# Performance work log

Measured on AMD Instinct MI355X. Metric: run time of the kernel, lower is better.

The kernel has to match this reference:

```python
import jax, jax.numpy as jnp
import numpy as np
from jax.scipy.special import logsumexp

REG_E = 0.05      # entropic regularization (init_kwargs reg_e)
N_ITER = 100      # n_iter_sinkhorn
N, M = 4096, 4096


def setup_inputs() -> dict:
    key = jax.random.key(0)
    k1, k2, k3 = jax.random.split(key, 3)
    p = jax.random.uniform(k1, (N,), dtype=jnp.float32)
    p = p / p.sum()                      # probability weights of measure P
    q = jax.random.uniform(k2, (M,), dtype=jnp.float32)
    q = q / q.sum()                      # probability weights of measure Q
    C = jax.random.uniform(k3, (N, M), dtype=jnp.float32)  # ground cost
    return {"p": p, "q": q, "C": C}


def reference(p, q, C):
    # POT ot.bregman.sinkhorn(..., method='sinkhorn_log') on C / C.max()
    # Log-domain Sinkhorn: Mr = -(C/max(C))/reg; alternate potential updates
    #   u = log p - logsumexp(Mr + v[None,:], axis=1)
    #   v = log q - logsumexp(Mr + u[:,None], axis=0)
    # plan = exp(Mr + u[:,None] + v[None,:])
    Mr = -(C / jax.lax.stop_gradient(jnp.max(C))) / REG_E   # (n, m)
    logp = jnp.log(p)
    logq = jnp.log(q)

    def body(_, uv):
        u, v = uv
        u = logp - logsumexp(Mr + v[None, :], axis=1)   # row logsumexp
        v = logq - logsumexp(Mr + u[:, None], axis=0)   # col logsumexp
        return (u, v)

    u0 = jnp.zeros_like(p)
    v0 = jnp.zeros_like(q)
    u, v = jax.lax.fori_loop(0, N_ITER, body, (u0, v0))
    return jnp.exp(Mr + u[:, None] + v[None, :])        # OT plan (n, m)
```

## Files before the change

### kernel.cpp

```cpp
#include <hip/hip_runtime.h>

#define N 4096
#define NITER 100
#define DSTEP (20.0f / 65535.0f)
#define LOG2E 1.44269504088896340736f
#define DSTEP2 (DSTEP * LOG2E)
#define TOL 3e-4f
#define NB 256
#define NT 1024
#define ROWS 16
#define TILE_BYTES (ROWS * N * 2)

typedef unsigned short u16;

__device__ __forceinline__ float aload(const float* p) {
    return __hip_atomic_load(p, __ATOMIC_RELAXED, __HIP_MEMORY_SCOPE_AGENT);
}
__device__ __forceinline__ void astore(float* p, float x) {
    __hip_atomic_store(p, x, __ATOMIC_RELAXED, __HIP_MEMORY_SCOPE_AGENT);
}
__device__ __forceinline__ int aloadi(const int* p) {
    return __hip_atomic_load(p, __ATOMIC_RELAXED, __HIP_MEMORY_SCOPE_AGENT);
}

__device__ __forceinline__ float fexp2(float x) {
#if __has_builtin(__builtin_amdgcn_exp2f)
    return __builtin_amdgcn_exp2f(x);
#else
    return __expf(x * 0.6931471805599453f);
#endif
}

__device__ __forceinline__ void gbar(int* bar, int slot) {
    __syncthreads();
    if (threadIdx.x == 0) {
        __hip_atomic_fetch_add(&bar[slot], 1, __ATOMIC_RELEASE, __HIP_MEMORY_SCOPE_AGENT);
        while (__hip_atomic_load(&bar[slot], __ATOMIC_ACQUIRE, __HIP_MEMORY_SCOPE_AGENT) < NB)
            __builtin_amdgcn_s_sleep(1);
    }
    __syncthreads();
}

__global__ __launch_bounds__(NT) void ot_all(const float* __restrict__ p,
                                             const float* __restrict__ q,
                                             const float* __restrict__ C,
                                             int* maxC,
                                             int* bar,
                                             float* v,
                                             float* part,
                                             float* ddel,
                                             float* __restrict__ out) {
    extern __shared__ u16 tile[];
    const int t = threadIdx.x;
    const int b = blockIdx.x;
    const int lane = t & 63;
    const int wave = t >> 6;
    const int gid = b * NT + t;
    const int r0 = b * ROWS;
    const int c0 = b * 16;
    const int j0 = t * 4;
    int slot = 0;

    __shared__ float sred[4][16];
    __shared__ float wbc[4];
    __shared__ float s2[16][16];
    __shared__ float dm[16];
    __shared__ float wm[16];
    __shared__ float lp[ROWS], pp[ROWS], lq[16], su[ROWS];

    {
        const float4* Crow = (const float4*)(C + (size_t)r0 * N);
        float m = 0.f;
        for (int i = t; i < ROWS * N / 4; i += NT) {
            float4 c = Crow[i];
            m = fmaxf(m, fmaxf(fmaxf(c.x, c.y), fmaxf(c.z, c.w)));
        }
#pragma unroll
        for (int off = 32; off; off >>= 1) m = fmaxf(m, __shfl_down(m, off));
        if (lane == 0) wm[wave] = m;
        __syncthreads();
        if (t == 0) {
            m = wm[0];
#pragma unroll
            for (int i = 1; i < 16; ++i) m = fmaxf(m, wm[i]);
            atomicMax(maxC, __float_as_int(m));
        }
    }
    gbar(bar, slot++);
    const float qmul = 65535.0f / __int_as_float(aloadi(maxC));

    {
        const float4* Crow = (const float4*)(C + (size_t)r0 * N);
        uint2* T2 = (uint2*)tile;
        for (int i = t; i < ROWS * N / 4; i += NT) {
            float4 a = Crow[i];
            uint2 o;
            o.x = min(65535u, __float2uint_rn(a.x * qmul)) | (min(65535u, __float2uint_rn(a.y * qmul)) << 16);
            o.y = min(65535u, __float2uint_rn(a.z * qmul)) | (min(65535u, __float2uint_rn(a.w * qmul)) << 16);
            T2[i] = o;
        }
        if (t < ROWS) {
            float pv = p[r0 + t];
            pp[t] = pv;
            lp[t] = __logf(pv);
            lq[t] = __logf(q[c0 + t]);
            su[t] = 0.f;
        }
        if (gid < N) astore(&v[gid], 0.f);
    }
    float vreg = 0.f;
    gbar(bar, slot++);

    for (int it = 0; it < NITER; ++it) {
        float vv2[4];
#pragma unroll
        for (int k = 0; k < 4; ++k) vv2[k] = aload(&v[j0 + k]) * LOG2E;
        float ca[4] = {0.f, 0.f, 0.f, 0.f};

        for (int ch = 0; ch < 4; ++ch) {
            const int rl = ch * 4;
            float tq[4][4], sp[4];
#pragma unroll
            for (int r = 0; r < 4; ++r) {
                uint2 a = *(const uint2*)(tile + (size_t)(rl + r) * N + j0);
                float e0 = fexp2(fmaf((float)(a.x & 0xffffu), -DSTEP2, vv2[0]));
                float e1 = fexp2(fmaf((float)(a.x >> 16),     -DSTEP2, vv2[1]));
                float e2 = fexp2(fmaf((float)(a.y & 0xffffu), -DSTEP2, vv2[2]));
                float e3 = fexp2(fmaf((float)(a.y >> 16),     -DSTEP2, vv2[3]));
                tq[r][0] = e0; tq[r][1] = e1; tq[r][2] = e2; tq[r][3] = e3;
                sp[r] = (e0 + e1) + (e2 + e3);
            }
#pragma unroll
            for (int r = 0; r < 4; ++r) {
                float s = sp[r];
#pragma unroll
                for (int off = 32; off; off >>= 1) s += __shfl_down(s, off);
                if (lane == 0) sred[r][wave] = s;
            }
            __syncthreads();
            if (wave < 4) {
                float s = (lane < 16) ? sred[wave][lane] : 0.f;
                s += __shfl_down(s, 8);
                s += __shfl_down(s, 4);
                s += __shfl_down(s, 2);
                s += __shfl_down(s, 1);
                if (lane == 0) {
                    wbc[wave] = pp[rl + wave] / s;
                    su[rl + wave] = lp[rl + wave] - __logf(s);
                }
            }
            __syncthreads();
#pragma unroll
            for (int r = 0; r < 4; ++r) {
                const float w = wbc[r];
#pragma unroll
                for (int k = 0; k < 4; ++k) ca[k] = fmaf(tq[r][k], w, ca[k]);
            }
        }
#pragma unroll
        for (int k = 0; k < 4; ++k) astore(&part[(size_t)b * N + j0 + k], ca[k]);
        gbar(bar, slot++);

        {
            const int cl = t & 15;
            const int ch = t >> 4;
            const int c = c0 + cl;
            float s = 0.f;
#pragma unroll
            for (int k = 0; k < 4; ++k) s += aload(&part[(size_t)(ch + 64 * k) * N + c]);
            s += __shfl_down(s, 16);
            s += __shfl_down(s, 32);
            if (lane < 16) s2[cl][wave] = s;
            __syncthreads();
            if (t < 16) {
                float tot = 0.f;
#pragma unroll
                for (int w = 0; w < 16; ++w) tot += s2[t][w];
                const float vn = lq[t] + vreg - __logf(tot);
                astore(&v[c0 + t], vn);
                float d = fabsf(vn - vreg);
                vreg = vn;
                d = fmaxf(d, __shfl_down(d, 8));
                d = fmaxf(d, __shfl_down(d, 4));
                d = fmaxf(d, __shfl_down(d, 2));
                d = fmaxf(d, __shfl_down(d, 1));
                if (t == 0) astore(&ddel[b], d);
            }
        }
        gbar(bar, slot++);

        {
            float d = aload(&ddel[t & 255]);
#pragma unroll
            for (int off = 32; off; off >>= 1) d = fmaxf(d, __shfl_down(d, off));
            if (lane == 0) dm[wave] = d;
            __syncthreads();
            float m = dm[0];
#pragma unroll
            for (int w = 1; w < 16; ++w) m = fmaxf(m, dm[w]);
            __syncthreads();
            if (m < TOL) break;
        }
    }

    {
        float vvl[4];
#pragma unroll
        for (int k = 0; k < 4; ++k) vvl[k] = aload(&v[j0 + k]) * LOG2E;
#pragma unroll 4
        for (int r = 0; r < ROWS; ++r) {
            const float uul = su[r] * LOG2E;
            uint2 a = *(const uint2*)(tile + (size_t)r * N + j0);
            float4 o;
            o.x = fexp2(fmaf((float)(a.x & 0xffffu), -DSTEP2, uul + vvl[0]));
            o.y = fexp2(fmaf((float)(a.x >> 16),     -DSTEP2, uul + vvl[1]));
            o.z = fexp2(fmaf((float)(a.y & 0xffffu), -DSTEP2, uul + vvl[2]));
            o.w = fexp2(fmaf((float)(a.y >> 16),     -DSTEP2, uul + vvl[3]));
            *(float4*)(out + (size_t)(r0 + r) * N + j0) = o;
        }
    }
}

extern "C" void kernel_launch(void* const* d_in, const int* in_sizes, int n_in,
                              void* d_out, int out_size, void* d_ws, size_t ws_size,
                              hipStream_t stream) {
    const float* p = (const float*)d_in[0];
    const float* q = (const float*)d_in[1];
    const float* C = (const float*)d_in[2];
    float* out = (float*)d_out;

    float* W = (float*)d_ws;
    int* maxC = (int*)W;
    int* bar = (int*)(W + 16);
    float* v = W + 512;
    float* ddel = v + N;
    float* part = (float*)((char*)d_ws + 128 * 1024);

    hipMemsetAsync(d_ws, 0, 2048, stream);

    hipFuncSetAttribute((const void*)ot_all, hipFuncAttributeMaxDynamicSharedMemorySize, TILE_BYTES);

    void* args[] = {(void*)&p, (void*)&q, (void*)&C, (void*)&maxC, (void*)&bar,
                    (void*)&v, (void*)&part, (void*)&ddel, (void*)&out};
    hipLaunchCooperativeKernel((void*)ot_all, dim3(NB), dim3(NT), args, TILE_BYTES, stream);
}
```

Before: 205.9 us.

## Use hierarchical grid barriers and overlap max-reduction with tile quantization

Replaces the flat single-counter grid barrier with a two-level barrier: blocks arrive on per-group counters and the last arriver of each group bumps a root counter. Every barrier event now gets its own counters, so the per-iteration ddel slots need no reuse hazard. The first barrier is split into arrive and wait so each block can quantize its C rows with its local max while other blocks finish. The global max is folded into the dequantization step afterwards. This also trims some intra-block syncs in the convergence check, at the cost of a larger workspace memset and more counter memory.

```diff
diff --git a/kernel.cpp b/kernel.cpp
--- a/kernel.cpp
+++ b/kernel.cpp
@@ -2,14 +2,15 @@
 
 #define N 4096
 #define NITER 100
-#define DSTEP (20.0f / 65535.0f)
 #define LOG2E 1.44269504088896340736f
-#define DSTEP2 (DSTEP * LOG2E)
 #define TOL 3e-4f
 #define NB 256
 #define NT 1024
 #define ROWS 16
 #define TILE_BYTES (ROWS * N * 2)
+#define GRPS 8
+#define BPG 32
+#define EVSTRIDE 144
 
 typedef unsigned short u16;
 
@@ -18,9 +19,6 @@
 }
 __device__ __forceinline__ void astore(float* p, float x) {
     __hip_atomic_store(p, x, __ATOMIC_RELAXED, __HIP_MEMORY_SCOPE_AGENT);
-}
-__device__ __forceinline__ int aloadi(const int* p) {
-    return __hip_atomic_load(p, __ATOMIC_RELAXED, __HIP_MEMORY_SCOPE_AGENT);
 }
 
 __device__ __forceinline__ float fexp2(float x) {
@@ -31,24 +29,32 @@
 #endif
 }
 
-__device__ __forceinline__ void gbar(int* bar, int slot) {
-    __syncthreads();
-    if (threadIdx.x == 0) {
-        __hip_atomic_fetch_add(&bar[slot], 1, __ATOMIC_RELEASE, __HIP_MEMORY_SCOPE_AGENT);
-        while (__hip_atomic_load(&bar[slot], __ATOMIC_ACQUIRE, __HIP_MEMORY_SCOPE_AGENT) < NB)
-            __builtin_amdgcn_s_sleep(1);
-    }
+__device__ __forceinline__ void gbar_arrive(int* bar, int e) {
+    int* base = bar + e * EVSTRIDE;
+    const int g = (int)(blockIdx.x >> 5);
+    int r = __hip_atomic_fetch_add(base + g * 16, 1, __ATOMIC_ACQ_REL, __HIP_MEMORY_SCOPE_AGENT);
+    if (r == BPG - 1)
+        __hip_atomic_fetch_add(base + 128, 1, __ATOMIC_ACQ_REL, __HIP_MEMORY_SCOPE_AGENT);
+}
+__device__ __forceinline__ void gbar_wait(int* bar, int e) {
+    const int* root = bar + e * EVSTRIDE + 128;
+    while (__hip_atomic_load(root, __ATOMIC_ACQUIRE, __HIP_MEMORY_SCOPE_AGENT) < GRPS)
+        __builtin_amdgcn_s_sleep(1);
+}
+__device__ __forceinline__ void gbar(int* bar, int e) {
+    __syncthreads();
+    if (threadIdx.x == 0) { gbar_arrive(bar, e); gbar_wait(bar, e); }
     __syncthreads();
 }
 
 __global__ __launch_bounds__(NT) void ot_all(const float* __restrict__ p,
                                              const float* __restrict__ q,
                                              const float* __restrict__ C,
-                                             int* maxC,
                                              int* bar,
+                                             float* fmax_arr,
+                                             float* ddel,
                                              float* v,
                                              float* part,
-                                             float* ddel,
                                              float* __restrict__ out) {
     extern __shared__ u16 tile[];
     const int t = threadIdx.x;
@@ -59,15 +65,15 @@
     const int r0 = b * ROWS;
     const int c0 = b * 16;
     const int j0 = t * 4;
-    int slot = 0;
 
     __shared__ float sred[4][16];
     __shared__ float wbc[4];
     __shared__ float s2[16][16];
     __shared__ float dm[16];
-    __shared__ float wm[16];
     __shared__ float lp[ROWS], pp[ROWS], lq[16], su[ROWS];
-
+    __shared__ float sMown, sMaxC, sM;
+
+    if (gid < N) astore(&v[gid], 0.f);
     {
         const float4* Crow = (const float4*)(C + (size_t)r0 * N);
         float m = 0.f;
@@ -77,19 +83,21 @@
         }
 #pragma unroll
         for (int off = 32; off; off >>= 1) m = fmaxf(m, __shfl_down(m, off));
-        if (lane == 0) wm[wave] = m;
+        if (lane == 0) dm[wave] = m;
         __syncthreads();
         if (t == 0) {
-            m = wm[0];
-#pragma unroll
-            for (int i = 1; i < 16; ++i) m = fmaxf(m, wm[i]);
-            atomicMax(maxC, __float_as_int(m));
-        }
-    }
-    gbar(bar, slot++);
-    const float qmul = 65535.0f / __int_as_float(aloadi(maxC));
+            m = dm[0];
+#pragma unroll
+            for (int i = 1; i < 16; ++i) m = fmaxf(m, dm[i]);
+            sMown = m;
+            astore(&fmax_arr[b], m);
+            gbar_arrive(bar, 0);
+        }
+        __syncthreads();
+    }
 
     {
+        const float qmul = 65535.0f / sMown;
         const float4* Crow = (const float4*)(C + (size_t)r0 * N);
         uint2* T2 = (uint2*)tile;
         for (int i = t; i < ROWS * N / 4; i += NT) {
@@ -106,10 +114,20 @@
             lq[t] = __logf(q[c0 + t]);
             su[t] = 0.f;
         }
-        if (gid < N) astore(&v[gid], 0.f);
-    }
+    }
+    __syncthreads();
+    if (t == 0) gbar_wait(bar, 0);
+    __syncthreads();
+    if (wave == 0) {
+        float d = fmaxf(fmaxf(aload(&fmax_arr[lane]), aload(&fmax_arr[64 + lane])),
+                        fmaxf(aload(&fmax_arr[128 + lane]), aload(&fmax_arr[192 + lane])));
+#pragma unroll
+        for (int off = 32; off; off >>= 1) d = fmaxf(d, __shfl_down(d, off));
+        if (lane == 0) sMaxC = d;
+    }
+    __syncthreads();
+    const float ndstep = -(20.0f / 65535.0f) * (sMown / sMaxC) * LOG2E;
     float vreg = 0.f;
-    gbar(bar, slot++);
 
     for (int it = 0; it < NITER; ++it) {
         float vv2[4];
@@ -123,10 +141,10 @@
 #pragma unroll
             for (int r = 0; r < 4; ++r) {
                 uint2 a = *(const uint2*)(tile + (size_t)(rl + r) * N + j0);
-                float e0 = fexp2(fmaf((float)(a.x & 0xffffu), -DSTEP2, vv2[0]));
-                float e1 = fexp2(fmaf((float)(a.x >> 16),     -DSTEP2, vv2[1]));
-                float e2 = fexp2(fmaf((float)(a.y & 0xffffu), -DSTEP2, vv2[2]));
-                float e3 = fexp2(fmaf((float)(a.y >> 16),     -DSTEP2, vv2[3]));
+                float e0 = fexp2(fmaf((float)(a.x & 0xffffu), ndstep, vv2[0]));
+                float e1 = fexp2(fmaf((float)(a.x >> 16),     ndstep, vv2[1]));
+                float e2 = fexp2(fmaf((float)(a.y & 0xffffu), ndstep, vv2[2]));
+                float e3 = fexp2(fmaf((float)(a.y >> 16),     ndstep, vv2[3]));
                 tq[r][0] = e0; tq[r][1] = e1; tq[r][2] = e2; tq[r][3] = e3;
                 sp[r] = (e0 + e1) + (e2 + e3);
             }
@@ -159,7 +177,7 @@
         }
 #pragma unroll
         for (int k = 0; k < 4; ++k) astore(&part[(size_t)b * N + j0 + k], ca[k]);
-        gbar(bar, slot++);
+        gbar(bar, 1 + 2 * it);
 
         {
             const int cl = t & 15;
@@ -184,23 +202,21 @@
                 d = fmaxf(d, __shfl_down(d, 4));
                 d = fmaxf(d, __shfl_down(d, 2));
                 d = fmaxf(d, __shfl_down(d, 1));
-                if (t == 0) astore(&ddel[b], d);
-            }
-        }
-        gbar(bar, slot++);
-
-        {
-            float d = aload(&ddel[t & 255]);
+                if (t == 0) astore(&ddel[it * NB + b], d);
+            }
+        }
+        gbar(bar, 2 + 2 * it);
+
+        if (wave == 0) {
+            const float* dd = ddel + it * NB;
+            float d = fmaxf(fmaxf(aload(dd + lane), aload(dd + 64 + lane)),
+                            fmaxf(aload(dd + 128 + lane), aload(dd + 192 + lane)));
 #pragma unroll
             for (int off = 32; off; off >>= 1) d = fmaxf(d, __shfl_down(d, off));
-            if (lane == 0) dm[wave] = d;
-            __syncthreads();
-            float m = dm[0];
-#pragma unroll
-            for (int w = 1; w < 16; ++w) m = fmaxf(m, dm[w]);
-            __syncthreads();
-            if (m < TOL) break;
-        }
+            if (lane == 0) sM = d;
+        }
+        __syncthreads();
+        if (sM < TOL) break;
     }
 
     {
@@ -212,10 +228,10 @@
             const float uul = su[r] * LOG2E;
             uint2 a = *(const uint2*)(tile + (size_t)r * N + j0);
             float4 o;
-            o.x = fexp2(fmaf((float)(a.x & 0xffffu), -DSTEP2, uul + vvl[0]));
-            o.y = fexp2(fmaf((float)(a.x >> 16),     -DSTEP2, uul + vvl[1]));
-            o.z = fexp2(fmaf((float)(a.y & 0xffffu), -DSTEP2, uul + vvl[2]));
-            o.w = fexp2(fmaf((float)(a.y >> 16),     -DSTEP2, uul + vvl[3]));
+            o.x = fexp2(fmaf((float)(a.x & 0xffffu), ndstep, uul + vvl[0]));
+            o.y = fexp2(fmaf((float)(a.x >> 16),     ndstep, uul + vvl[1]));
+            o.z = fexp2(fmaf((float)(a.y & 0xffffu), ndstep, uul + vvl[2]));
+            o.w = fexp2(fmaf((float)(a.y >> 16),     ndstep, uul + vvl[3]));
             *(float4*)(out + (size_t)(r0 + r) * N + j0) = o;
         }
     }
@@ -229,18 +245,18 @@
     const float* C = (const float*)d_in[2];
     float* out = (float*)d_out;
 
-    float* W = (float*)d_ws;
-    int* maxC = (int*)W;
-    int* bar = (int*)(W + 16);
-    float* v = W + 512;
-    float* ddel = v + N;
-    float* part = (float*)((char*)d_ws + 128 * 1024);
-
-    hipMemsetAsync(d_ws, 0, 2048, stream);
+    char* base = (char*)d_ws;
+    int* bar = (int*)base;
+    float* fmax_arr = (float*)(base + 120 * 1024);
+    float* ddel = (float*)(base + 124 * 1024);
+    float* v = (float*)(base + 228 * 1024);
+    float* part = (float*)(base + 256 * 1024);
+
+    hipMemsetAsync(d_ws, 0, (size_t)(1 + 2 * NITER) * EVSTRIDE * sizeof(int), stream);
 
     hipFuncSetAttribute((const void*)ot_all, hipFuncAttributeMaxDynamicSharedMemorySize, TILE_BYTES);
 
-    void* args[] = {(void*)&p, (void*)&q, (void*)&C, (void*)&maxC, (void*)&bar,
-                    (void*)&v, (void*)&part, (void*)&ddel, (void*)&out};
+    void* args[] = {(void*)&p, (void*)&q, (void*)&C, (void*)&bar,
+                    (void*)&fmax_arr, (void*)&ddel, (void*)&v, (void*)&part, (void*)&out};
     hipLaunchCooperativeKernel((void*)ot_all, dim3(NB), dim3(NT), args, TILE_BYTES, stream);
 }
```

After: 210.3 us. +2.1%, slower.
